# Kernel tuning notes

Hardware: AMD Instinct MI355X
Metric: run time of the kernel (lower is better)

## Reference

```python
import jax, jax.numpy as jnp
import numpy as np

N_BOND = 2_000_000
N_ATOM = 100_000
N_STRUCT = 2
THREEBODY_CUTOFF = 0.8


def setup_inputs() -> dict:
    key = jax.random.key(0)
    k1, k2 = jax.random.split(key)
    # bonds grouped (sorted) by source atom, as _compute_threebody assumes
    bond_src = jnp.sort(jax.random.randint(k1, (N_BOND,), 0, N_ATOM))
    bond_length = jax.random.uniform(k2, (N_BOND,), dtype=jnp.float32)
    n_atoms = jnp.full((N_STRUCT,), N_ATOM // N_STRUCT, dtype=jnp.int32)
    return {"bond_src": bond_src, "bond_length": bond_length, "n_atoms": n_atoms}


def reference(bond_src, bond_length, n_atoms):
    """Vectorized equivalent of compute_threebody_indices.

    Returns (bond_indices [T,2] pairs of ORIGINAL bond ids, n_triple_ij [n_bond],
    n_triple_i [n_atom], n_triple_s [n_struct]). Replaces the O(n) Python loops
    with segment-sum (degree count), prefix-sum (CSR offsets) and a flat
    enumeration of ordered within-atom bond pairs (j != k).
    """
    n_bond = bond_src.shape[0]
    n_atom = int(jnp.sum(n_atoms))
    n_struct = n_atoms.shape[0]

    # --- filter bonds by three-body cutoff, remember original bond ids ---
    mask = bond_length <= THREEBODY_CUTOFF
    kept = jnp.nonzero(mask)[0]          # original bond indices of surviving bonds
    src = bond_src[kept]                 # still sorted (subset of a sorted array)

    # --- per-atom bond counts and CSR offsets (parallel histogram + scan) ---
    deg = jax.ops.segment_sum(jnp.ones_like(src), src, num_segments=n_atom)
    bond_offset = jnp.cumsum(deg) - deg  # start of each atom's bond block

    # --- triples per atom / per bond / per structure ---
    n_triple_i = deg * (deg - 1)
    T = int(jnp.sum(n_triple_i))

    # --- enumerate all ordered pairs (j, k), j != k, within each atom block ---
    tri_atom = jnp.repeat(jnp.arange(n_atom), n_triple_i, total_repeat_length=T)
    tri_start = (jnp.cumsum(n_triple_i) - n_triple_i)[tri_atom]
    t = jnp.arange(T) - tri_start        # local triple index in [0, d*(d-1))
    d = deg[tri_atom]                    # d >= 2 wherever triples exist
    j = t // (d - 1)
    kp = t % (d - 1)
    k = kp + (kp >= j).astype(kp.dtype)  # skip k == j, preserving loop order
    b0 = bond_offset[tri_atom] + j       # relative (filtered) bond index
    b1 = bond_offset[tri_atom] + k
    bond_indices = jnp.stack([kept[b0], kept[b1]], axis=1)  # back to ORIGINAL ids

    # angles per ORIGINAL bond: deg(src)-1 for surviving bonds, 0 for filtered
    n_triple_ij = jnp.zeros(n_bond, dtype=deg.dtype).at[kept].set(deg[src] - 1)

    # angles per structure
    struct_id = jnp.repeat(jnp.arange(n_struct), n_atoms, total_repeat_length=n_atom)
    n_triple_s = jax.ops.segment_sum(n_triple_i, struct_id, num_segments=n_struct)

    return bond_indices, n_triple_ij, n_triple_i, n_triple_s
```

## Files before the change

### kernel.cpp

```cpp
#include <hip/hip_runtime.h>


#define CUTOFF 0.8f
#define NATOM_C 100000
#define MAXD 256

__global__ void k0_init(int* wstart, int* wend, int n_atom) {
    int i = blockIdx.x * blockDim.x + threadIdx.x;
    if (i < n_atom) { wstart[i] = 0; wend[i] = 0; }
}

__global__ void k1_bounds(const int* __restrict__ src, int* wstart, int* wend, int n_bond) {
    int i = blockIdx.x * blockDim.x + threadIdx.x;
    if (i >= n_bond) return;
    int a = src[i];
    if (i == 0 || src[i - 1] != a) wstart[a] = i;
    if (i == n_bond - 1 || src[i + 1] != a) wend[a] = i + 1;
}

__global__ void k2_deg(const float* __restrict__ len, const int* __restrict__ wstart,
                       const int* __restrict__ wend, int* __restrict__ deg,
                       int* __restrict__ out_i, int n_atom) {
    int gid = blockIdx.x * blockDim.x + threadIdx.x;
    int a = gid >> 6;
    int lane = threadIdx.x & 63;
    if (a >= n_atom) return;
    int s = wstart[a], e = wend[a];
    int d = 0;
    for (int base = s; base < e; base += 64) {
        int idx = base + lane;
        bool m = (idx < e) && (len[idx] <= CUTOFF);
        d += __popcll(__ballot(m));
    }
    if (lane == 0) { deg[a] = d; out_i[a] = d * (d - 1); }
}

__global__ void k3a_scan(const int* __restrict__ vals, int* __restrict__ exsc,
                         int* __restrict__ bsums, int n) {
    __shared__ int tmp[256];
    int t = threadIdx.x;
    int base = blockIdx.x * 1024 + t * 4;
    int v0 = 0, v1 = 0, v2 = 0, v3 = 0;
    if (base     < n) v0 = vals[base];
    if (base + 1 < n) v1 = vals[base + 1];
    if (base + 2 < n) v2 = vals[base + 2];
    if (base + 3 < n) v3 = vals[base + 3];
    int s = v0 + v1 + v2 + v3;
    tmp[t] = s;
    __syncthreads();
    for (int off = 1; off < 256; off <<= 1) {
        int v = (t >= off) ? tmp[t - off] : 0;
        __syncthreads();
        tmp[t] += v;
        __syncthreads();
    }
    int excl = tmp[t] - s;
    if (base     < n) exsc[base]     = excl;
    if (base + 1 < n) exsc[base + 1] = excl + v0;
    if (base + 2 < n) exsc[base + 2] = excl + v0 + v1;
    if (base + 3 < n) exsc[base + 3] = excl + v0 + v1 + v2;
    if (t == 255) bsums[blockIdx.x] = tmp[255];
}

__global__ void k3b_scan(int* __restrict__ bsums, int* __restrict__ total, int nb) {
    const int B = 256;
    __shared__ int sums[B];
    int t = threadIdx.x;
    int chunk = (nb + B - 1) / B;
    int lo = t * chunk; if (lo > nb) lo = nb;
    int hi = lo + chunk; if (hi > nb) hi = nb;
    int ssum = 0;
    for (int i = lo; i < hi; i++) ssum += bsums[i];
    sums[t] = ssum;
    __syncthreads();
    for (int off = 1; off < B; off <<= 1) {
        int v = (t >= off) ? sums[t - off] : 0;
        __syncthreads();
        sums[t] += v;
        __syncthreads();
    }
    int run = sums[t] - ssum;
    for (int i = lo; i < hi; i++) { int v = bsums[i]; bsums[i] = run; run += v; }
    if (t == B - 1) *total = sums[B - 1];
}

__global__ void k3c_add(int* __restrict__ exsc, const int* __restrict__ bsums, int n) {
    int i = blockIdx.x * blockDim.x + threadIdx.x;
    if (i < n) exsc[i] += bsums[i >> 10];
}

__global__ void k5_enum(const float* __restrict__ len, const int* __restrict__ wstart,
                        const int* __restrict__ wend, const int* __restrict__ tstart,
                        int2* __restrict__ out_pairs, int* __restrict__ out_ij,
                        int n_atom) {
    __shared__ int kept[4 * MAXD];
    int wave = threadIdx.x >> 6;
    int lane = threadIdx.x & 63;
    int a = blockIdx.x * 4 + wave;
    int* my = &kept[wave * MAXD];
    int d = 0;
    int s = 0, e = 0;
    if (a < n_atom) {
        s = wstart[a]; e = wend[a];
        for (int base = s; base < e; base += 64) {
            int idx = base + lane;
            bool m = (idx < e) && (len[idx] <= CUTOFF);
            unsigned long long bal = __ballot(m);
            int pos = d + __popcll(bal & ((1ull << lane) - 1ull));
            if (m && pos < MAXD) my[pos] = idx;
            d += __popcll(bal);
        }
        int dm1 = d - 1;
        for (int idx = s + lane; idx < e; idx += 64)
            out_ij[idx] = (len[idx] <= CUTOFF) ? dm1 : 0;
    }
    __syncthreads();
    if (a < n_atom && d >= 2) {
        int dm1 = d - 1;
        int nT = d * dm1;
        int base_row = tstart[a];
        for (int t = lane; t < nT; t += 64) {
            int j = t / dm1;
            int kp = t - j * dm1;
            int k = kp + (kp >= j ? 1 : 0);
            out_pairs[base_row + t] = make_int2(my[j], my[k]);
        }
    }
}

__global__ void k6_struct(const int* __restrict__ n_atoms_arr, const int* __restrict__ tstart,
                          int* __restrict__ out_s, int n_struct) {
    if (blockIdx.x == 0 && threadIdx.x == 0) {
        int off = 0;
        for (int s = 0; s < n_struct; s++) {
            int c = n_atoms_arr[s];
            out_s[s] = tstart[off + c] - tstart[off];
            off += c;
        }
    }
}

extern "C" void kernel_launch(void* const* d_in, const int* in_sizes, int n_in,
                              void* d_out, int out_size, void* d_ws, size_t ws_size,
                              hipStream_t stream) {
    const int*   bond_src    = (const int*)d_in[0];
    const float* bond_len    = (const float*)d_in[1];
    const int*   n_atoms_arr = (const int*)d_in[2];
    int n_bond   = in_sizes[0];
    int n_struct = in_sizes[2];
    const int n_atom = NATOM_C;
    int T2 = out_size - n_bond - n_atom - n_struct;

    int nblk_scan = (n_atom + 1023) / 1024;

    int* ws     = (int*)d_ws;
    int* wstart = ws;
    int* wend   = ws + n_atom;
    int* deg    = ws + 2 * n_atom;
    int* tstart = ws + 3 * n_atom;
    int* bsums  = tstart + n_atom + 1;

    int*  out       = (int*)d_out;
    int2* out_pairs = (int2*)out;
    int*  out_ij    = out + T2;
    int*  out_i     = out_ij + n_bond;
    int*  out_s     = out_i + n_atom;

    k0_init  <<<(n_atom + 255) / 256, 256, 0, stream>>>(wstart, wend, n_atom);
    k1_bounds<<<(n_bond + 255) / 256, 256, 0, stream>>>(bond_src, wstart, wend, n_bond);
    k2_deg   <<<(n_atom * 64 + 255) / 256, 256, 0, stream>>>(bond_len, wstart, wend, deg, out_i, n_atom);
    k3a_scan <<<nblk_scan, 256, 0, stream>>>(out_i, tstart, bsums, n_atom);
    k3b_scan <<<1, 256, 0, stream>>>(bsums, tstart + n_atom, nblk_scan);
    k3c_add  <<<(n_atom + 255) / 256, 256, 0, stream>>>(tstart, bsums, n_atom);
    k5_enum  <<<(n_atom + 3) / 4, 256, 0, stream>>>(bond_len, wstart, wend, tstart, out_pairs, out_ij, n_atom);
    k6_struct<<<1, 1, 0, stream>>>(n_atoms_arr, tstart, out_s, n_struct);
}
```

Baseline: 273.5 us.

## Fuse degree counting into bounds kernel and vectorize triple pair stores

```diff
diff --git a/kernel.cpp b/kernel.cpp
--- a/kernel.cpp
+++ b/kernel.cpp
@@ -5,46 +5,50 @@
 #define NATOM_C 100000
 #define MAXD 256
 
-__global__ void k0_init(int* wstart, int* wend, int n_atom) {
+__global__ void k0_init(int* wstart, int* wend, int* deg, int n_atom) {
     int i = blockIdx.x * blockDim.x + threadIdx.x;
-    if (i < n_atom) { wstart[i] = 0; wend[i] = 0; }
+    if (i < n_atom) { wstart[i] = 0; wend[i] = 0; deg[i] = 0; }
 }
 
-__global__ void k1_bounds(const int* __restrict__ src, int* wstart, int* wend, int n_bond) {
+__global__ void kA_bounds_deg(const int* __restrict__ src, const float* __restrict__ len,
+                              int* __restrict__ wstart, int* __restrict__ wend,
+                              int* __restrict__ deg, int n_bond) {
     int i = blockIdx.x * blockDim.x + threadIdx.x;
-    if (i >= n_bond) return;
-    int a = src[i];
-    if (i == 0 || src[i - 1] != a) wstart[a] = i;
-    if (i == n_bond - 1 || src[i + 1] != a) wend[a] = i + 1;
+    int lane = threadIdx.x & 63;
+    bool valid = i < n_bond;
+    int a = -1;
+    bool kept = false;
+    if (valid) {
+        a = src[i];
+        if (i == 0 || src[i - 1] != a) wstart[a] = i;
+        if (i == n_bond - 1 || src[i + 1] != a) wend[a] = i + 1;
+        kept = (len[i] <= CUTOFF);
+    }
+    unsigned long long keptB = __ballot(kept);
+    int ap = __shfl_up(a, 1);
+    bool head = (lane == 0) || (ap != a);
+    unsigned long long headB = __ballot(head);
+    unsigned long long nextHeads = (headB >> 1) >> lane;
+    bool tail = (lane == 63) || ((nextHeads & 1ull) != 0ull);
+    if (tail && valid) {
+        unsigned long long below = (lane == 63) ? ~0ull : ((2ull << lane) - 1ull);
+        int runStart = 63 - __clzll(headB & below);
+        unsigned long long runMask = below & ~((1ull << runStart) - 1ull);
+        int cnt = __popcll(keptB & runMask);
+        if (cnt) atomicAdd(&deg[a], cnt);
+    }
 }
 
-__global__ void k2_deg(const float* __restrict__ len, const int* __restrict__ wstart,
-                       const int* __restrict__ wend, int* __restrict__ deg,
-                       int* __restrict__ out_i, int n_atom) {
-    int gid = blockIdx.x * blockDim.x + threadIdx.x;
-    int a = gid >> 6;
-    int lane = threadIdx.x & 63;
-    if (a >= n_atom) return;
-    int s = wstart[a], e = wend[a];
-    int d = 0;
-    for (int base = s; base < e; base += 64) {
-        int idx = base + lane;
-        bool m = (idx < e) && (len[idx] <= CUTOFF);
-        d += __popcll(__ballot(m));
-    }
-    if (lane == 0) { deg[a] = d; out_i[a] = d * (d - 1); }
-}
-
-__global__ void k3a_scan(const int* __restrict__ vals, int* __restrict__ exsc,
-                         int* __restrict__ bsums, int n) {
+__global__ void kB_scan(const int* __restrict__ deg, int* __restrict__ out_i,
+                        int* __restrict__ exsc, int* __restrict__ bsums, int n) {
     __shared__ int tmp[256];
     int t = threadIdx.x;
     int base = blockIdx.x * 1024 + t * 4;
     int v0 = 0, v1 = 0, v2 = 0, v3 = 0;
-    if (base     < n) v0 = vals[base];
-    if (base + 1 < n) v1 = vals[base + 1];
-    if (base + 2 < n) v2 = vals[base + 2];
-    if (base + 3 < n) v3 = vals[base + 3];
+    if (base     < n) { int d = deg[base];     v0 = d * (d - 1); out_i[base]     = v0; }
+    if (base + 1 < n) { int d = deg[base + 1]; v1 = d * (d - 1); out_i[base + 1] = v1; }
+    if (base + 2 < n) { int d = deg[base + 2]; v2 = d * (d - 1); out_i[base + 2] = v2; }
+    if (base + 3 < n) { int d = deg[base + 3]; v3 = d * (d - 1); out_i[base + 3] = v3; }
     int s = v0 + v1 + v2 + v3;
     tmp[t] = s;
     __syncthreads();
@@ -62,7 +66,9 @@
     if (t == 255) bsums[blockIdx.x] = tmp[255];
 }
 
-__global__ void k3b_scan(int* __restrict__ bsums, int* __restrict__ total, int nb) {
+__global__ void kC_scan2(int* __restrict__ bsums, const int* __restrict__ exsc,
+                         const int* __restrict__ n_atoms_arr, int* __restrict__ out_s,
+                         int nb, int n_atom, int n_struct) {
     const int B = 256;
     __shared__ int sums[B];
     int t = threadIdx.x;
@@ -81,25 +87,30 @@
     }
     int run = sums[t] - ssum;
     for (int i = lo; i < hi; i++) { int v = bsums[i]; bsums[i] = run; run += v; }
-    if (t == B - 1) *total = sums[B - 1];
+    int total = sums[B - 1];
+    __syncthreads();
+    if (t == 0) {
+        int off = 0, prevA = 0;
+        for (int s = 0; s < n_struct; s++) {
+            off += n_atoms_arr[s];
+            int A = (off >= n_atom) ? total : (exsc[off] + bsums[off >> 10]);
+            out_s[s] = A - prevA;
+            prevA = A;
+        }
+    }
 }
 
-__global__ void k3c_add(int* __restrict__ exsc, const int* __restrict__ bsums, int n) {
-    int i = blockIdx.x * blockDim.x + threadIdx.x;
-    if (i < n) exsc[i] += bsums[i >> 10];
-}
-
-__global__ void k5_enum(const float* __restrict__ len, const int* __restrict__ wstart,
-                        const int* __restrict__ wend, const int* __restrict__ tstart,
-                        int2* __restrict__ out_pairs, int* __restrict__ out_ij,
+__global__ void kD_enum(const float* __restrict__ len, const int* __restrict__ wstart,
+                        const int* __restrict__ wend, const int* __restrict__ exsc,
+                        const int* __restrict__ bsums,
+                        int4* __restrict__ out4, int* __restrict__ out_ij,
                         int n_atom) {
-    __shared__ int kept[4 * MAXD];
+    __shared__ int keptIds[4 * MAXD];
     int wave = threadIdx.x >> 6;
     int lane = threadIdx.x & 63;
     int a = blockIdx.x * 4 + wave;
-    int* my = &kept[wave * MAXD];
-    int d = 0;
-    int s = 0, e = 0;
+    int* my = &keptIds[wave * MAXD];
+    int d = 0, s = 0, e = 0;
     if (a < n_atom) {
         s = wstart[a]; e = wend[a];
         for (int base = s; base < e; base += 64) {
@@ -116,26 +127,19 @@
     }
     __syncthreads();
     if (a < n_atom && d >= 2) {
-        int dm1 = d - 1;
-        int nT = d * dm1;
-        int base_row = tstart[a];
-        for (int t = lane; t < nT; t += 64) {
-            int j = t / dm1;
-            int kp = t - j * dm1;
-            int k = kp + (kp >= j ? 1 : 0);
-            out_pairs[base_row + t] = make_int2(my[j], my[k]);
-        }
-    }
-}
-
-__global__ void k6_struct(const int* __restrict__ n_atoms_arr, const int* __restrict__ tstart,
-                          int* __restrict__ out_s, int n_struct) {
-    if (blockIdx.x == 0 && threadIdx.x == 0) {
-        int off = 0;
-        for (int s = 0; s < n_struct; s++) {
-            int c = n_atoms_arr[s];
-            out_s[s] = tstart[off + c] - tstart[off];
-            off += c;
+        unsigned dm1 = (unsigned)(d - 1);
+        unsigned nP = ((unsigned)(d * (d - 1))) >> 1;
+        int base_row = exsc[a] + bsums[a >> 10];
+        int b4 = base_row >> 1;
+        for (unsigned p = lane; p < nP; p += 64) {
+            unsigned t0 = 2u * p;
+            unsigned j  = t0 / dm1;
+            unsigned kp = t0 - j * dm1;
+            unsigned j1 = j, kp1 = kp + 1;
+            if (kp1 == dm1) { j1++; kp1 = 0; }
+            unsigned k0 = kp  + (kp  >= j  ? 1u : 0u);
+            unsigned k1 = kp1 + (kp1 >= j1 ? 1u : 0u);
+            out4[b4 + p] = make_int4(my[j], my[k0], my[j1], my[k1]);
         }
     }
 }
@@ -157,21 +161,18 @@
     int* wstart = ws;
     int* wend   = ws + n_atom;
     int* deg    = ws + 2 * n_atom;
-    int* tstart = ws + 3 * n_atom;
-    int* bsums  = tstart + n_atom + 1;
+    int* exsc   = ws + 3 * n_atom;
+    int* bsums  = exsc + n_atom;
 
     int*  out       = (int*)d_out;
-    int2* out_pairs = (int2*)out;
+    int4* out_pairs = (int4*)out;
     int*  out_ij    = out + T2;
     int*  out_i     = out_ij + n_bond;
     int*  out_s     = out_i + n_atom;
 
-    k0_init  <<<(n_atom + 255) / 256, 256, 0, stream>>>(wstart, wend, n_atom);
-    k1_bounds<<<(n_bond + 255) / 256, 256, 0, stream>>>(bond_src, wstart, wend, n_bond);
-    k2_deg   <<<(n_atom * 64 + 255) / 256, 256, 0, stream>>>(bond_len, wstart, wend, deg, out_i, n_atom);
-    k3a_scan <<<nblk_scan, 256, 0, stream>>>(out_i, tstart, bsums, n_atom);
-    k3b_scan <<<1, 256, 0, stream>>>(bsums, tstart + n_atom, nblk_scan);
-    k3c_add  <<<(n_atom + 255) / 256, 256, 0, stream>>>(tstart, bsums, n_atom);
-    k5_enum  <<<(n_atom + 3) / 4, 256, 0, stream>>>(bond_len, wstart, wend, tstart, out_pairs, out_ij, n_atom);
-    k6_struct<<<1, 1, 0, stream>>>(n_atoms_arr, tstart, out_s, n_struct);
+    k0_init      <<<(n_atom + 255) / 256, 256, 0, stream>>>(wstart, wend, deg, n_atom);
+    kA_bounds_deg<<<(n_bond + 255) / 256, 256, 0, stream>>>(bond_src, bond_len, wstart, wend, deg, n_bond);
+    kB_scan      <<<nblk_scan, 256, 0, stream>>>(deg, out_i, exsc, bsums, n_atom);
+    kC_scan2     <<<1, 256, 0, stream>>>(bsums, exsc, n_atoms_arr, out_s, nblk_scan, n_atom, n_struct);
+    kD_enum      <<<(n_atom + 3) / 4, 256, 0, stream>>>(bond_len, wstart, wend, exsc, bsums, out_pairs, out_ij, n_atom);
 }
```

Result: faster. 244.1 us (-10.7%).
